# Performance work log

Hardware: AMD Instinct MI355X
Metric: run time of the kernel (lower is better)

Reference implementation:

```python
import jax, jax.numpy as jnp
import numpy as np

N_NODES = 50000
N_EDGES = 500000
F_DIM = 128
N_REL = 8
N_LAYERS = 2
NEG_SLOPE = 0.2  # PyG RGATConv default negative_slope


def setup_inputs() -> dict:
    key = jax.random.key(0)
    ks = jax.random.split(key, 6)
    x = jax.random.normal(ks[0], (N_NODES, F_DIM), dtype=jnp.float32)
    edge_index = jax.random.randint(ks[1], (2, N_EDGES), 0, N_NODES)
    edge_type = jax.random.randint(ks[2], (N_EDGES,), 0, N_REL)
    # Per-layer relation weights [L, R, F_in, F_out], attention vectors q,k [L, F_out, 1], bias [L, F_out]
    W = jax.random.normal(ks[3], (N_LAYERS, N_REL, F_DIM, F_DIM), dtype=jnp.float32) * (1.0 / np.sqrt(F_DIM)).astype(np.float32)
    att_q = jax.random.normal(ks[4], (N_LAYERS, F_DIM, 1), dtype=jnp.float32) * 0.1
    att_k = jax.random.normal(ks[5], (N_LAYERS, F_DIM, 1), dtype=jnp.float32) * 0.1
    bias = jnp.zeros((N_LAYERS, F_DIM), dtype=jnp.float32)
    return {"x": x, "W": W, "att_q": att_q, "att_k": att_k, "bias": bias,
            "edge_index": edge_index, "edge_type": edge_type}


def _segment_softmax(logits, seg, num_segments):
    # Numerically stable softmax over edges grouped by destination node.
    m = jax.ops.segment_max(logits, seg, num_segments=num_segments)
    m = jax.lax.stop_gradient(m)
    e = jnp.exp(logits - m[seg])
    denom = jax.ops.segment_sum(e, seg, num_segments=num_segments)
    return e / (denom[seg] + 1e-16)


def _rgat_layer(h, src, dst, edge_type, W, q, k, b):
    # h: [N, F]; W: [R, F, F]. Project once per relation, then gather per edge
    # (avoids materializing [E, F, F] per-edge weight gathers).
    n = h.shape[0]
    xw = jnp.einsum('nf,rfg->rng', h, W)          # [R, N, F]
    out_j = xw[edge_type, src]                    # [E, F] transformed source feats
    out_i = xw[edge_type, dst]                    # [E, F] transformed dest feats
    # additive self-attention: leaky_relu(q(x_i) + k(x_j)), heads=1, dim=1
    logits = jax.nn.leaky_relu((out_i @ q + out_j @ k)[:, 0], NEG_SLOPE)  # [E]
    alpha = _segment_softmax(logits, dst, n)      # across-relation softmax per dst node
    agg = jax.ops.segment_sum(alpha[:, None] * out_j, dst, num_segments=n)  # [N, F]
    return agg + b


def reference(x, W, att_q, att_k, bias, edge_index, edge_type):
    src, dst = edge_index[0], edge_index[1]
    h = x
    for l in range(W.shape[0]):  # small fixed layer count
        h = _rgat_layer(h, src, dst, edge_type, W[l], att_q[l], att_k[l], bias[l])
        h = jax.nn.relu(h)  # dropout is identity in eval mode
    return h
```

## Files before the change

### kernel.cpp

```cpp
#include <hip/hip_runtime.h>
#include <hip/hip_bf16.h>
#include <hip/hip_fp16.h>

#define N_NODES 50000
#define N_EDGES 500000
#define F_DIM   128
#define N_REL   8
#define N_LAYERS 2
#define NEG_SLOPE 0.2f

#define NBLK_N ((N_NODES + 255) / 256)

typedef _Float16 half8 __attribute__((ext_vector_type(8)));
typedef float f32x4  __attribute__((ext_vector_type(4)));


__device__ inline float lrelu(float l) { return (l > 0.f) ? l : NEG_SLOPE * l; }

__global__ __launch_bounds__(256) void prep_h(const float* __restrict__ H,
                                              _Float16* __restrict__ Hf) {
    const size_t i8 = (size_t)blockIdx.x * 256 + threadIdx.x;
    if (i8 >= (size_t)N_NODES * F_DIM / 8) return;
    const float* src = H + i8 * 8;
    float av[8];
    *(float4*)(av)     = *(const float4*)(src);
    *(float4*)(av + 4) = *(const float4*)(src + 4);
    alignas(16) _Float16 hb[8];
#pragma unroll
    for (int j = 0; j < 8; ++j) hb[j] = (_Float16)av[j];
    *(uint4*)(Hf + i8 * 8) = *(const uint4*)hb;
}

__global__ __launch_bounds__(256) void prep_w(const float* __restrict__ W,
                                              _Float16* __restrict__ Wf) {
    __shared__ float tile[64][F_DIM + 1];
    const int mat = blockIdx.x;
    const float* src = W + (size_t)mat * F_DIM * F_DIM;
    const int t = threadIdx.x;
    for (int hf = 0; hf < 2; ++hf) {
#pragma unroll
        for (int i = 0; i < 8; ++i) {
            int idx = t + i * 256;
            int f = idx >> 5, c4 = idx & 31;
            float4 v = *(const float4*)(src + (size_t)(hf * 64 + f) * F_DIM + c4 * 4);
            *(float4*)&tile[f][c4 * 4] = v;
        }
        __syncthreads();
        int g = t >> 1, fs = (t & 1) * 32;
        for (int c = 0; c < 4; ++c) {
            alignas(16) _Float16 th[8];
#pragma unroll
            for (int j = 0; j < 8; ++j) th[j] = (_Float16)tile[fs + c * 8 + j][g];
            size_t o = ((size_t)mat * F_DIM + g) * F_DIM + hf * 64 + fs + c * 8;
            *(uint4*)(Wf + o) = *(const uint4*)th;
        }
        __syncthreads();
    }
}

#define GBM 128
#define RGRP 2
__global__ __launch_bounds__(256, 2) void gemm_xw(const _Float16* __restrict__ Hf,
                                                  const _Float16* __restrict__ Wf,
                                                  const float* __restrict__ qv_g,
                                                  const float* __restrict__ kv_g,
                                                  __half* __restrict__ xw,
                                                  float* __restrict__ a_q,
                                                  float* __restrict__ a_k) {
    __shared__ _Float16 lds[F_DIM * F_DIM];
    const int rb0 = blockIdx.x * GBM;
    const int r0  = blockIdx.y * RGRP;
    const int tid = threadIdx.x;
    const int lane = tid & 63, w = tid >> 6;
    const int q = lane >> 4, ln = lane & 15;

    half8 Af[2][4];
#pragma unroll
    for (int rt = 0; rt < 2; ++rt) {
        int row = rb0 + w * 32 + rt * 16 + ln;
        int ar = (row < N_NODES) ? row : (N_NODES - 1);
        const _Float16* hp = Hf + (size_t)ar * F_DIM;
#pragma unroll
        for (int ks = 0; ks < 4; ++ks)
            Af[rt][ks] = *(const half8*)(hp + ks * 32 + q * 8);
    }

    float qvl[8], kvl[8];
#pragma unroll
    for (int t = 0; t < 8; ++t) {
        qvl[t] = qv_g[t * 16 + ln];
        kvl[t] = kv_g[t * 16 + ln];
    }

    for (int rr = 0; rr < RGRP; ++rr) {
        const int r = r0 + rr;
        __syncthreads();
        {
            const _Float16* src = Wf + (size_t)r * F_DIM * F_DIM;
#pragma unroll
            for (int i = 0; i < 8; ++i) {
                int chunk = tid + i * 256;
                int gg = chunk >> 4, c8 = chunk & 15;
                uint4 v = *(const uint4*)(src + gg * F_DIM + c8 * 8);
                *(uint4*)(lds + gg * F_DIM + ((c8 ^ (gg & 15)) * 8)) = v;
            }
        }
        __syncthreads();

        f32x4 acc[2][8];
#pragma unroll
        for (int rt = 0; rt < 2; ++rt)
#pragma unroll
            for (int t = 0; t < 8; ++t) acc[rt][t] = (f32x4)(0.f);

#pragma unroll
        for (int ks = 0; ks < 4; ++ks) {
            const int jx = (((ks * 4 + q) ^ ln)) << 3;
            half8 Bf[8];
#pragma unroll
            for (int c = 0; c < 8; ++c)
                Bf[c] = *(const half8*)(lds + (c * 16 + ln) * F_DIM + jx);
#pragma unroll
            for (int c = 0; c < 8; ++c)
#pragma unroll
                for (int rt = 0; rt < 2; ++rt)
                    acc[rt][c] = __builtin_amdgcn_mfma_f32_16x16x32_f16(Af[rt][ks], Bf[c], acc[rt][c], 0, 0, 0);
        }

#pragma unroll
        for (int rt = 0; rt < 2; ++rt) {
            float pq[4], pk[4];
#pragma unroll
            for (int reg = 0; reg < 4; ++reg) {
                const int row = rb0 + w * 32 + rt * 16 + q * 4 + reg;
                alignas(16) unsigned short hs[8];
                float sq = 0.f, sk = 0.f;
#pragma unroll
                for (int t = 0; t < 8; ++t) {
                    float v = acc[rt][t][reg];
                    __half hv = __float2half(v);
                    hs[t] = *reinterpret_cast<unsigned short*>(&hv);
                    sq = fmaf(v, qvl[t], sq);
                    sk = fmaf(v, kvl[t], sk);
                }
                if (row < N_NODES)
                    *(uint4*)(xw + ((size_t)r * N_NODES + row) * F_DIM + ln * 8) = *(const uint4*)hs;
                pq[reg] = sq; pk[reg] = sk;
            }
#pragma unroll
            for (int reg = 0; reg < 4; ++reg) {
#pragma unroll
                for (int m = 1; m <= 8; m <<= 1) {
                    pq[reg] += __shfl_xor(pq[reg], m);
                    pk[reg] += __shfl_xor(pk[reg], m);
                }
            }
            if (ln == 0) {
#pragma unroll
                for (int reg = 0; reg < 4; ++reg) {
                    const int row = rb0 + w * 32 + rt * 16 + q * 4 + reg;
                    if (row < N_NODES) {
                        a_q[r * N_NODES + row] = pq[reg];
                        a_k[r * N_NODES + row] = pk[reg];
                    }
                }
            }
        }
    }
}


__global__ __launch_bounds__(256) void count_kernel(const int* __restrict__ dstp,
                                                    int* __restrict__ cnt) {
    int e = blockIdx.x * 256 + threadIdx.x;
    if (e < N_EDGES) atomicAdd(cnt + dstp[e], 1);
}

__global__ __launch_bounds__(256) void block_sum_kernel(const int* __restrict__ cnt,
                                                        int* __restrict__ partial) {
    __shared__ int s[256];
    int idx = blockIdx.x * 256 + threadIdx.x;
    int v = (idx < N_NODES) ? cnt[idx] : 0;
    s[threadIdx.x] = v;
    __syncthreads();
    for (int off = 128; off > 0; off >>= 1) {
        if (threadIdx.x < off) s[threadIdx.x] += s[threadIdx.x + off];
        __syncthreads();
    }
    if (threadIdx.x == 0) partial[blockIdx.x] = s[0];
}

__global__ __launch_bounds__(256) void scan_partials_kernel(int* __restrict__ partial,
                                                            int* __restrict__ row_ptr) {
    __shared__ int s[256];
    int t = threadIdx.x;
    int v = (t < NBLK_N) ? partial[t] : 0;
    s[t] = v;
    __syncthreads();
#pragma unroll
    for (int off = 1; off < 256; off <<= 1) {
        int x = (t >= off) ? s[t - off] : 0;
        __syncthreads();
        s[t] += x;
        __syncthreads();
    }
    if (t < NBLK_N) partial[t] = s[t] - v;
    if (t == 0) row_ptr[N_NODES] = N_EDGES;
}

__global__ __launch_bounds__(256) void scan_block_kernel(const int* __restrict__ cnt,
                                                         const int* __restrict__ partial,
                                                         int* __restrict__ row_ptr) {
    __shared__ int s[256];
    int t = threadIdx.x;
    int idx = blockIdx.x * 256 + t;
    int v = (idx < N_NODES) ? cnt[idx] : 0;
    s[t] = v;
    __syncthreads();
#pragma unroll
    for (int off = 1; off < 256; off <<= 1) {
        int x = (t >= off) ? s[t - off] : 0;
        __syncthreads();
        s[t] += x;
        __syncthreads();
    }
    if (idx < N_NODES) row_ptr[idx] = partial[blockIdx.x] + s[t] - v;
}

__global__ __launch_bounds__(256) void scatter_kernel(const int* __restrict__ srcp,
                                                      const int* __restrict__ dstp,
                                                      const int* __restrict__ etp,
                                                      const int* __restrict__ row_ptr,
                                                      int* __restrict__ cursor,
                                                      unsigned* __restrict__ sorted) {
    int e = blockIdx.x * 256 + threadIdx.x;
    if (e >= N_EDGES) return;
    int d = dstp[e];
    int pos = atomicAdd(cursor + d, 1);
    sorted[row_ptr[d] + pos] = (unsigned)srcp[e] | ((unsigned)etp[e] << 16);
}

__device__ inline void accum8(float* acc, uint4 v, float a) {
    const __half2* h2 = reinterpret_cast<const __half2*>(&v);
#pragma unroll
    for (int t = 0; t < 4; ++t) {
        float2 f = __half22float2(h2[t]);
        acc[t * 2]     = fmaf(a, f.x, acc[t * 2]);
        acc[t * 2 + 1] = fmaf(a, f.y, acc[t * 2 + 1]);
    }
}
__device__ inline const uint4* xwrow(const __half* xw, unsigned p, int ln) {
    return (const uint4*)(xw + (((size_t)(p >> 16)) * N_NODES + (p & 0xffff)) * F_DIM + ln * 8);
}

__global__ __launch_bounds__(256) void agg_fused(const __half* __restrict__ xw,
                                                 const float* __restrict__ a_q,
                                                 const float* __restrict__ a_k,
                                                 const int* __restrict__ row_ptr,
                                                 const unsigned* __restrict__ sorted,
                                                 const float* __restrict__ bias,
                                                 float* __restrict__ outp,
                                                 _Float16* __restrict__ hfp) {
    const int lane = threadIdx.x & 63;
    const int wave = threadIdx.x >> 6;
    const int d = blockIdx.x * 4 + wave;
    if (d >= N_NODES) return;
    const int beg = row_ptr[d], end = row_ptr[d + 1];
    const int cnt = end - beg;
    const int g = lane >> 4, ln = lane & 15;

    if (cnt <= 64) {
        unsigned p = 0;
        float l = -3.4e38f;
        if (lane < cnt) {
            p = sorted[beg + lane];
            int s = p & 0xffff, t = p >> 16;
            l = lrelu(a_q[t * N_NODES + d] + a_k[t * N_NODES + s]);
        }
        float m = l;
#pragma unroll
        for (int off = 32; off > 0; off >>= 1) m = fmaxf(m, __shfl_xor(m, off));
        float ex = (lane < cnt) ? __expf(l - m) : 0.f;
        float dsum = ex;
#pragma unroll
        for (int off = 32; off > 0; off >>= 1) dsum += __shfl_xor(dsum, off);
        const float alpha = ex / (dsum + 1e-16f);

        float acc[8] = {0, 0, 0, 0, 0, 0, 0, 0};
        for (int i = 0; i < cnt; i += 8) {
            unsigned p0 = __shfl(p, i + g);
            unsigned p1 = __shfl(p, i + 4 + g);
            float a0 = __shfl(alpha, i + g);
            float a1 = __shfl(alpha, i + 4 + g);
            uint4 v0 = *xwrow(xw, p0, ln);
            uint4 v1 = *xwrow(xw, p1, ln);
            accum8(acc, v0, a0);
            accum8(acc, v1, a1);
        }
#pragma unroll
        for (int t = 0; t < 8; ++t) {
            acc[t] += __shfl_xor(acc[t], 16);
            acc[t] += __shfl_xor(acc[t], 32);
        }
        if (g == 0) {
#pragma unroll
            for (int t = 0; t < 8; ++t) {
                const int col = t * 16 + ln;
                const float v = fmaxf(acc[t] + bias[col], 0.f);
                if (outp) outp[(size_t)d * F_DIM + col] = v;
                if (hfp)  hfp[(size_t)d * F_DIM + col] = (_Float16)v;
            }
        }
    } else {
        const int p0 = lane * 2;
        const int c0 = (p0 & 7) * 16 + (p0 >> 3);
        const int c1 = c0 + 16;
        float2 acc = make_float2(bias[c0], bias[c1]);
        float m = -3.4e38f;
        for (int i = beg + lane; i < end; i += 64) {
            unsigned p = sorted[i];
            int s = p & 0xffff, t = p >> 16;
            m = fmaxf(m, lrelu(a_q[t * N_NODES + d] + a_k[t * N_NODES + s]));
        }
#pragma unroll
        for (int off = 32; off > 0; off >>= 1) m = fmaxf(m, __shfl_xor(m, off));
        float dsum = 0.f;
        for (int i = beg + lane; i < end; i += 64) {
            unsigned p = sorted[i];
            int s = p & 0xffff, t = p >> 16;
            dsum += __expf(lrelu(a_q[t * N_NODES + d] + a_k[t * N_NODES + s]) - m);
        }
#pragma unroll
        for (int off = 32; off > 0; off >>= 1) dsum += __shfl_xor(dsum, off);
        const float inv = 1.f / (dsum + 1e-16f);
        for (int i = beg; i < end; ++i) {
            unsigned p = sorted[i];
            int s = p & 0xffff, t = p >> 16;
            float alpha = __expf(lrelu(a_q[t * N_NODES + d] + a_k[t * N_NODES + s]) - m) * inv;
            const __half2 h2 = *((const __half2*)xw + (((size_t)(p >> 16)) * N_NODES + (p & 0xffff)) * (F_DIM / 2) + lane);
            float2 v = make_float2(__half2float(h2.x), __half2float(h2.y));
            acc.x = fmaf(alpha, v.x, acc.x);
            acc.y = fmaf(alpha, v.y, acc.y);
        }
        const float v0 = fmaxf(acc.x, 0.f), v1 = fmaxf(acc.y, 0.f);
        if (outp) { outp[(size_t)d * F_DIM + c0] = v0; outp[(size_t)d * F_DIM + c1] = v1; }
        if (hfp)  { hfp[(size_t)d * F_DIM + c0] = (_Float16)v0; hfp[(size_t)d * F_DIM + c1] = (_Float16)v1; }
    }
}


extern "C" void kernel_launch(void* const* d_in, const int* in_sizes, int n_in,
                              void* d_out, int out_size, void* d_ws, size_t ws_size,
                              hipStream_t stream) {
    const float* x     = (const float*)d_in[0];
    const float* W     = (const float*)d_in[1];
    const float* att_q = (const float*)d_in[2];
    const float* att_k = (const float*)d_in[3];
    const float* bias  = (const float*)d_in[4];
    const int* ei      = (const int*)d_in[5];
    const int* etp     = (const int*)d_in[6];
    const int* srcp = ei;
    const int* dstp = ei + N_EDGES;
    float* out = (float*)d_out;
    char* ws   = (char*)d_ws;

    size_t off = 0;
    auto alloc = [&](size_t bytes) {
        void* p = ws + off;
        off = (off + bytes + 511) & ~(size_t)511;
        return p;
    };
    __half* xw       = (__half*)alloc((size_t)N_REL * N_NODES * F_DIM * sizeof(__half));
    float* a_q       = (float*)alloc((size_t)N_REL * N_NODES * sizeof(float));
    float* a_k       = (float*)alloc((size_t)N_REL * N_NODES * sizeof(float));
    int* cnt         = (int*)alloc((size_t)2 * N_NODES * sizeof(int));
    int* cursor      = cnt + N_NODES;
    int* row_ptr     = (int*)alloc(((size_t)N_NODES + 1) * sizeof(int));
    int* partial     = (int*)alloc(256 * sizeof(int));
    unsigned* sorted = (unsigned*)alloc((size_t)N_EDGES * sizeof(unsigned));
    _Float16* Wf     = (_Float16*)alloc((size_t)N_LAYERS * N_REL * F_DIM * F_DIM * sizeof(_Float16));
    _Float16* Hf     = (_Float16*)alloc((size_t)N_NODES * F_DIM * sizeof(_Float16));

    prep_w<<<N_LAYERS * N_REL, 256, 0, stream>>>(W, Wf);
    hipMemsetAsync(cnt, 0, (size_t)2 * N_NODES * 4, stream);
    count_kernel<<<(N_EDGES + 255) / 256, 256, 0, stream>>>(dstp, cnt);
    block_sum_kernel<<<NBLK_N, 256, 0, stream>>>(cnt, partial);
    scan_partials_kernel<<<1, 256, 0, stream>>>(partial, row_ptr);
    scan_block_kernel<<<NBLK_N, 256, 0, stream>>>(cnt, partial, row_ptr);
    scatter_kernel<<<(N_EDGES + 255) / 256, 256, 0, stream>>>(
        srcp, dstp, etp, row_ptr, cursor, sorted);

    const int grid_h = (N_NODES * F_DIM / 8 + 255) / 256;
    const int grid_m = (N_NODES + GBM - 1) / GBM;
    prep_h<<<grid_h, 256, 0, stream>>>(x, Hf);
    for (int l = 0; l < N_LAYERS; ++l) {
        gemm_xw<<<dim3(grid_m, N_REL / RGRP), 256, 0, stream>>>(
            Hf, Wf + (size_t)l * N_REL * F_DIM * F_DIM,
            att_q + l * F_DIM, att_k + l * F_DIM,
            xw, a_q, a_k);
        const bool last = (l == N_LAYERS - 1);
        agg_fused<<<(N_NODES + 3) / 4, 256, 0, stream>>>(
            xw, a_q, a_k, row_ptr, sorted, bias + l * F_DIM,
            last ? out : nullptr,
            last ? nullptr : Hf);
    }
}
```

Measured before the change: 300.9 us.

## Precompute per-edge attention logits in a separate kernel and defer softmax normalization

The per-node attention scalars a_q and a_k now use a node-major layout, and a new logits_kernel computes every edge's leaky-ReLU logit once into a CSR-ordered array. It uses a 16-bit destination array written by the scatter step. The aggregation kernel reads these precomputed logits instead of doing random a_q/a_k gathers. For short neighbor lists it unrolls the gather loop to four rows per iteration and applies the softmax denominator once at the end, so the reduction no longer sits ahead of the loads. The cost is an extra kernel launch per layer plus extra edge-sized buffers to write and read.

```diff
diff --git a/kernel.cpp b/kernel.cpp
--- a/kernel.cpp
+++ b/kernel.cpp
@@ -160,8 +160,8 @@
                 for (int reg = 0; reg < 4; ++reg) {
                     const int row = rb0 + w * 32 + rt * 16 + q * 4 + reg;
                     if (row < N_NODES) {
-                        a_q[r * N_NODES + row] = pq[reg];
-                        a_k[r * N_NODES + row] = pk[reg];
+                        a_q[(size_t)row * N_REL + r] = pq[reg];
+                        a_k[(size_t)row * N_REL + r] = pk[reg];
                     }
                 }
             }
@@ -232,12 +232,28 @@
                                                       const int* __restrict__ etp,
                                                       const int* __restrict__ row_ptr,
                                                       int* __restrict__ cursor,
-                                                      unsigned* __restrict__ sorted) {
+                                                      unsigned* __restrict__ sorted,
+                                                      unsigned short* __restrict__ dst16) {
     int e = blockIdx.x * 256 + threadIdx.x;
     if (e >= N_EDGES) return;
     int d = dstp[e];
     int pos = atomicAdd(cursor + d, 1);
-    sorted[row_ptr[d] + pos] = (unsigned)srcp[e] | ((unsigned)etp[e] << 16);
+    int j = row_ptr[d] + pos;
+    sorted[j] = (unsigned)srcp[e] | ((unsigned)etp[e] << 16);
+    dst16[j] = (unsigned short)d;
+}
+
+__global__ __launch_bounds__(256) void logits_kernel(const float* __restrict__ a_q,
+                                                     const float* __restrict__ a_k,
+                                                     const unsigned* __restrict__ sorted,
+                                                     const unsigned short* __restrict__ dst16,
+                                                     float* __restrict__ lgt) {
+    int j = blockIdx.x * 256 + threadIdx.x;
+    if (j >= N_EDGES) return;
+    unsigned p = sorted[j];
+    int s = p & 0xffff, t = p >> 16;
+    int d = dst16[j];
+    lgt[j] = lrelu(a_q[(size_t)d * N_REL + t] + a_k[(size_t)s * N_REL + t]);
 }
 
 __device__ inline void accum8(float* acc, uint4 v, float a) {
@@ -254,8 +270,7 @@
 }
 
 __global__ __launch_bounds__(256) void agg_fused(const __half* __restrict__ xw,
-                                                 const float* __restrict__ a_q,
-                                                 const float* __restrict__ a_k,
+                                                 const float* __restrict__ lgt,
                                                  const int* __restrict__ row_ptr,
                                                  const unsigned* __restrict__ sorted,
                                                  const float* __restrict__ bias,
@@ -274,39 +289,43 @@
         float l = -3.4e38f;
         if (lane < cnt) {
             p = sorted[beg + lane];
-            int s = p & 0xffff, t = p >> 16;
-            l = lrelu(a_q[t * N_NODES + d] + a_k[t * N_NODES + s]);
+            l = lgt[beg + lane];
         }
         float m = l;
 #pragma unroll
         for (int off = 32; off > 0; off >>= 1) m = fmaxf(m, __shfl_xor(m, off));
-        float ex = (lane < cnt) ? __expf(l - m) : 0.f;
+        const float ex = (lane < cnt) ? __expf(l - m) : 0.f;
+
+        float acc[8] = {0, 0, 0, 0, 0, 0, 0, 0};
+        for (int i = 0; i < cnt; i += 16) {
+            const bool b1 = (i + 4) < cnt, b2 = (i + 8) < cnt, b3 = (i + 12) < cnt;
+            unsigned p0 = __shfl(p, i + g);
+            float a0 = __shfl(ex, i + g);
+            uint4 v0 = *xwrow(xw, p0, ln);
+            uint4 v1, v2, v3;
+            float a1 = 0.f, a2 = 0.f, a3 = 0.f;
+            if (b1) { unsigned q1 = __shfl(p, i + 4 + g);  a1 = __shfl(ex, i + 4 + g);  v1 = *xwrow(xw, q1, ln); }
+            if (b2) { unsigned q2 = __shfl(p, i + 8 + g);  a2 = __shfl(ex, i + 8 + g);  v2 = *xwrow(xw, q2, ln); }
+            if (b3) { unsigned q3 = __shfl(p, i + 12 + g); a3 = __shfl(ex, i + 12 + g); v3 = *xwrow(xw, q3, ln); }
+            accum8(acc, v0, a0);
+            if (b1) accum8(acc, v1, a1);
+            if (b2) accum8(acc, v2, a2);
+            if (b3) accum8(acc, v3, a3);
+        }
         float dsum = ex;
 #pragma unroll
         for (int off = 32; off > 0; off >>= 1) dsum += __shfl_xor(dsum, off);
-        const float alpha = ex / (dsum + 1e-16f);
-
-        float acc[8] = {0, 0, 0, 0, 0, 0, 0, 0};
-        for (int i = 0; i < cnt; i += 8) {
-            unsigned p0 = __shfl(p, i + g);
-            unsigned p1 = __shfl(p, i + 4 + g);
-            float a0 = __shfl(alpha, i + g);
-            float a1 = __shfl(alpha, i + 4 + g);
-            uint4 v0 = *xwrow(xw, p0, ln);
-            uint4 v1 = *xwrow(xw, p1, ln);
-            accum8(acc, v0, a0);
-            accum8(acc, v1, a1);
-        }
 #pragma unroll
         for (int t = 0; t < 8; ++t) {
             acc[t] += __shfl_xor(acc[t], 16);
             acc[t] += __shfl_xor(acc[t], 32);
         }
         if (g == 0) {
+            const float inv = 1.f / (dsum + 1e-16f);
 #pragma unroll
             for (int t = 0; t < 8; ++t) {
                 const int col = t * 16 + ln;
-                const float v = fmaxf(acc[t] + bias[col], 0.f);
+                const float v = fmaxf(fmaf(acc[t], inv, bias[col]), 0.f);
                 if (outp) outp[(size_t)d * F_DIM + col] = v;
                 if (hfp)  hfp[(size_t)d * F_DIM + col] = (_Float16)v;
             }
@@ -317,26 +336,17 @@
         const int c1 = c0 + 16;
         float2 acc = make_float2(bias[c0], bias[c1]);
         float m = -3.4e38f;
-        for (int i = beg + lane; i < end; i += 64) {
-            unsigned p = sorted[i];
-            int s = p & 0xffff, t = p >> 16;
-            m = fmaxf(m, lrelu(a_q[t * N_NODES + d] + a_k[t * N_NODES + s]));
-        }
+        for (int i = beg + lane; i < end; i += 64) m = fmaxf(m, lgt[i]);
 #pragma unroll
         for (int off = 32; off > 0; off >>= 1) m = fmaxf(m, __shfl_xor(m, off));
         float dsum = 0.f;
-        for (int i = beg + lane; i < end; i += 64) {
-            unsigned p = sorted[i];
-            int s = p & 0xffff, t = p >> 16;
-            dsum += __expf(lrelu(a_q[t * N_NODES + d] + a_k[t * N_NODES + s]) - m);
-        }
+        for (int i = beg + lane; i < end; i += 64) dsum += __expf(lgt[i] - m);
 #pragma unroll
         for (int off = 32; off > 0; off >>= 1) dsum += __shfl_xor(dsum, off);
         const float inv = 1.f / (dsum + 1e-16f);
         for (int i = beg; i < end; ++i) {
             unsigned p = sorted[i];
-            int s = p & 0xffff, t = p >> 16;
-            float alpha = __expf(lrelu(a_q[t * N_NODES + d] + a_k[t * N_NODES + s]) - m) * inv;
+            float alpha = __expf(lgt[i] - m) * inv;
             const __half2 h2 = *((const __half2*)xw + (((size_t)(p >> 16)) * N_NODES + (p & 0xffff)) * (F_DIM / 2) + lane);
             float2 v = make_float2(__half2float(h2.x), __half2float(h2.y));
             acc.x = fmaf(alpha, v.x, acc.x);
@@ -371,13 +381,15 @@
         return p;
     };
     __half* xw       = (__half*)alloc((size_t)N_REL * N_NODES * F_DIM * sizeof(__half));
-    float* a_q       = (float*)alloc((size_t)N_REL * N_NODES * sizeof(float));
-    float* a_k       = (float*)alloc((size_t)N_REL * N_NODES * sizeof(float));
+    float* a_q       = (float*)alloc((size_t)N_NODES * N_REL * sizeof(float));
+    float* a_k       = (float*)alloc((size_t)N_NODES * N_REL * sizeof(float));
     int* cnt         = (int*)alloc((size_t)2 * N_NODES * sizeof(int));
     int* cursor      = cnt + N_NODES;
     int* row_ptr     = (int*)alloc(((size_t)N_NODES + 1) * sizeof(int));
     int* partial     = (int*)alloc(256 * sizeof(int));
     unsigned* sorted = (unsigned*)alloc((size_t)N_EDGES * sizeof(unsigned));
+    unsigned short* dst16 = (unsigned short*)alloc((size_t)N_EDGES * sizeof(unsigned short));
+    float* lgt       = (float*)alloc((size_t)N_EDGES * sizeof(float));
     _Float16* Wf     = (_Float16*)alloc((size_t)N_LAYERS * N_REL * F_DIM * F_DIM * sizeof(_Float16));
     _Float16* Hf     = (_Float16*)alloc((size_t)N_NODES * F_DIM * sizeof(_Float16));
 
@@ -388,19 +400,21 @@
     scan_partials_kernel<<<1, 256, 0, stream>>>(partial, row_ptr);
     scan_block_kernel<<<NBLK_N, 256, 0, stream>>>(cnt, partial, row_ptr);
     scatter_kernel<<<(N_EDGES + 255) / 256, 256, 0, stream>>>(
-        srcp, dstp, etp, row_ptr, cursor, sorted);
+        srcp, dstp, etp, row_ptr, cursor, sorted, dst16);
 
     const int grid_h = (N_NODES * F_DIM / 8 + 255) / 256;
     const int grid_m = (N_NODES + GBM - 1) / GBM;
+    const int grid_e = (N_EDGES + 255) / 256;
     prep_h<<<grid_h, 256, 0, stream>>>(x, Hf);
     for (int l = 0; l < N_LAYERS; ++l) {
         gemm_xw<<<dim3(grid_m, N_REL / RGRP), 256, 0, stream>>>(
             Hf, Wf + (size_t)l * N_REL * F_DIM * F_DIM,
             att_q + l * F_DIM, att_k + l * F_DIM,
             xw, a_q, a_k);
+        logits_kernel<<<grid_e, 256, 0, stream>>>(a_q, a_k, sorted, dst16, lgt);
         const bool last = (l == N_LAYERS - 1);
         agg_fused<<<(N_NODES + 3) / 4, 256, 0, stream>>>(
-            xw, a_q, a_k, row_ptr, sorted, bias + l * F_DIM,
+            xw, lgt, row_ptr, sorted, bias + l * F_DIM,
             last ? out : nullptr,
             last ? nullptr : Hf);
     }
```

New measurement: 311.3 us. 3.5% more time.
